# Optimization experiments

Measured on AMD Instinct MI355X. Metric: run time of the kernel, lower is better.

Reference implementation:

```python
import jax, jax.numpy as jnp
import numpy as np

NEG = -1e30


def setup_inputs() -> dict:
    key = jax.random.key(0)
    ks = jax.random.split(key, 8)
    B, d, Lc, Lq = 32, 128, 2048, 512
    C = jax.random.normal(ks[0], (B, d, Lc), dtype=jnp.float32)
    Q = jax.random.normal(ks[1], (B, d, Lq), dtype=jnp.float32)
    Cmask = jax.random.randint(ks[2], (B, Lc), 0, 2, dtype=jnp.int32)
    Qmask = jax.random.randint(ks[3], (B, Lq), 0, 2, dtype=jnp.int32)
    # xavier_uniform over (d, 1): bound = sqrt(6 / (d + 1))
    bnd = float(np.sqrt(6.0 / (d + 1)))
    w_c = jax.random.uniform(ks[4], (d, 1), minval=-bnd, maxval=bnd, dtype=jnp.float32)
    w_q = jax.random.uniform(ks[5], (d, 1), minval=-bnd, maxval=bnd, dtype=jnp.float32)
    bnd_m = float(np.sqrt(6.0 / (1 + d)))
    w_mul = jax.random.uniform(ks[6], (1, 1, d), minval=-bnd_m, maxval=bnd_m, dtype=jnp.float32)
    bias = jnp.zeros((1,), dtype=jnp.float32)
    return {"C": C, "Q": Q, "Cmask": Cmask, "Qmask": Qmask,
            "w_c": w_c, "w_q": w_q, "w_mul": w_mul, "bias": bias}


def reference(C, Q, Cmask, Qmask, w_c, w_q, w_mul, bias):
    # C: [B, d, Lc], Q: [B, d, Lq] -> transpose to token-major
    Ct = jnp.swapaxes(C, 1, 2)  # [B, Lc, d]
    Qt = jnp.swapaxes(Q, 1, 2)  # [B, Lq, d]
    cm = Cmask.astype(jnp.float32)[:, :, None]   # [B, Lc, 1]
    qm = Qmask.astype(jnp.float32)[:, None, :]   # [B, 1, Lq]
    # optimized trilinear similarity S: [B, Lc, Lq] (dropout p=0 / eval mode)
    s0 = Ct @ w_c                                  # [B, Lc, 1]
    s1 = jnp.swapaxes(Qt @ w_q, 1, 2)              # [B, 1, Lq]
    s2 = jnp.einsum('bcd,bqd->bcq', Ct * w_mul, Qt)  # [B, Lc, Lq]
    S = s0 + s1 + s2 + bias
    S1 = jax.nn.softmax(S + NEG * (1.0 - qm), axis=2)  # mask over query axis
    S2 = jax.nn.softmax(S + NEG * (1.0 - cm), axis=1)  # mask over context axis
    A = jnp.einsum('bcq,bqd->bcd', S1, Qt)             # [B, Lc, d]
    Bm = jnp.einsum('bck,bkd->bcd', jnp.einsum('bcq,bkq->bck', S1, S2), Ct)
    out = jnp.concatenate([Ct, A, Ct * A, Ct * Bm], axis=2)  # [B, Lc, 4d]
    return jnp.swapaxes(out, 1, 2)  # [B, 4d, Lc]
```

## Files before the change

### kernel.cpp

```cpp
#include <hip/hip_runtime.h>

#define B_ 32
#define D_ 128
#define LC 2048
#define LQ 512
#define CCH 16

#define NEGINF (-3.0e38f)

typedef __attribute__((ext_vector_type(8))) short bf16x8;
typedef __attribute__((ext_vector_type(4))) float f32x4;
typedef __attribute__((ext_vector_type(8))) unsigned short us8;
typedef __attribute__((ext_vector_type(8))) _Float16 f16x8;

__device__ __forceinline__ unsigned short bf16rne(float x) {
    unsigned int u = __float_as_uint(x);
    u = (u + 0x7FFFu + ((u >> 16) & 1u)) >> 16;
    return (unsigned short)u;
}

__device__ __forceinline__ void gll16(const void* g, void* l) {
    __builtin_amdgcn_global_load_lds((const __attribute__((address_space(1))) void*)g,
                                     (__attribute__((address_space(3))) void*)l, 16, 0, 0);
}

__global__ void k_dotw(const float* __restrict__ X, const float* __restrict__ w,
                       float* __restrict__ outv, int L) {
    int idx = blockIdx.x * 256 + threadIdx.x;
    int b = idx / L, x = idx - b * L;
    const float* Xp = X + (size_t)b * D_ * L + x;
    float acc = 0.f;
#pragma unroll 8
    for (int dd = 0; dd < D_; ++dd) acc += Xp[(size_t)dd * L] * w[dd];
    outv[idx] = acc;
}

__global__ void k_prep_C(const float* __restrict__ C, const float* __restrict__ wmul,
                         short* __restrict__ Ctw, short* __restrict__ Cb16) {
    int b = blockIdx.y, c0 = blockIdx.x * 64;
    __shared__ float Tf[128][65];
    __shared__ float wm[128];
    int t = threadIdx.x;
    if (t < 128) wm[t] = wmul[t];
    const float* Cb = C + (size_t)b * D_ * LC;
#pragma unroll
    for (int i = 0; i < 8; ++i) {
        int idx = t + i * 256;
        int d = idx >> 4, c4 = idx & 15;
        float4 v = *(const float4*)(Cb + (size_t)d * LC + c0 + c4 * 4);
        Tf[d][c4 * 4 + 0] = v.x; Tf[d][c4 * 4 + 1] = v.y;
        Tf[d][c4 * 4 + 2] = v.z; Tf[d][c4 * 4 + 3] = v.w;
        ushort4 cv;
        cv.x = bf16rne(v.x); cv.y = bf16rne(v.y); cv.z = bf16rne(v.z); cv.w = bf16rne(v.w);
        *(ushort4*)(Cb16 + ((size_t)b * D_ + d) * LC + c0 + c4 * 4) = cv;
    }
    __syncthreads();
    int c_l = t & 63, g = t >> 6;
    unsigned short u[32];
#pragma unroll
    for (int j = 0; j < 32; ++j) {
        int d = g * 32 + j;
        u[j] = bf16rne(Tf[d][c_l] * wm[d]);
    }
    short* dst = Ctw + ((size_t)b * LC + c0 + c_l) * D_ + g * 32;
#pragma unroll
    for (int k = 0; k < 4; ++k) *(us8*)(dst + k * 8) = *(const us8*)&u[k * 8];
}

__global__ void k_prep_Q(const float* __restrict__ Q, short* __restrict__ Qt16,
                         short* __restrict__ Wf) {
    int b = blockIdx.y, q0 = blockIdx.x * 64;
    __shared__ float Tf[128][65];
    int t = threadIdx.x;
    const float* Qb = Q + (size_t)b * D_ * LQ;
#pragma unroll
    for (int i = 0; i < 8; ++i) {
        int idx = t + i * 256;
        int d = idx >> 4, q4 = idx & 15;
        float4 v = *(const float4*)(Qb + (size_t)d * LQ + q0 + q4 * 4);
        Tf[d][q4 * 4 + 0] = v.x; Tf[d][q4 * 4 + 1] = v.y;
        Tf[d][q4 * 4 + 2] = v.z; Tf[d][q4 * 4 + 3] = v.w;
        ushort4 cv;
        cv.x = bf16rne(v.x); cv.y = bf16rne(v.y); cv.z = bf16rne(v.z); cv.w = bf16rne(v.w);
        *(ushort4*)(Wf + ((size_t)b * 256 + d) * LQ + q0 + q4 * 4) = cv;
    }
    __syncthreads();
    int q_l = t & 63, g = t >> 6;
    unsigned short u[32];
#pragma unroll
    for (int j = 0; j < 32; ++j) u[j] = bf16rne(Tf[g * 32 + j][q_l]);
    short* dst = Qt16 + ((size_t)b * LQ + q0 + q_l) * D_ + g * 32;
#pragma unroll
    for (int k = 0; k < 4; ++k) *(us8*)(dst + k * 8) = *(const us8*)&u[k * 8];
}

__global__ __launch_bounds__(256) void k_S_mfma(const short* __restrict__ Ctw,
                                                const short* __restrict__ Qt16,
                                                const float* __restrict__ s0,
                                                const float* __restrict__ s1,
                                                const float* __restrict__ bias,
                                                const int* __restrict__ Cmask,
                                                _Float16* __restrict__ S16,
                                                float* __restrict__ pm,
                                                float* __restrict__ pl) {
    int b = blockIdx.y;
    int cT = blockIdx.x >> 2, qT = blockIdx.x & 3;
    int c0 = cT * 128, q0 = qT * 128;
    int t = threadIdx.x, w = t >> 6, l = t & 63;
    int wm_ = w >> 1, wn = w & 1;
    __shared__ short As[128 * 64];
    __shared__ short Bs[128 * 64];
    f32x4 acc[4][4] = {};
    const short* Arow = Ctw + ((size_t)b * LC + c0) * D_;
    const short* Brow = Qt16 + ((size_t)b * LQ + q0) * D_;
    int lr = l >> 3, sl = l & 7;
    for (int kt = 0; kt < 2; ++kt) {
        __syncthreads();
#pragma unroll
        for (int i = 0; i < 4; ++i) {
            int r = w * 32 + i * 8 + lr;
            int g = sl ^ (r & 7);
            gll16(Arow + (size_t)r * D_ + kt * 64 + g * 8, &As[(w * 32 + i * 8) * 64]);
            gll16(Brow + (size_t)r * D_ + kt * 64 + g * 8, &Bs[(w * 32 + i * 8) * 64]);
        }
        __syncthreads();
#pragma unroll
        for (int ks = 0; ks < 2; ++ks) {
            int kg = ks * 4 + (l >> 4);
            bf16x8 af[4], bfr[4];
#pragma unroll
            for (int ms = 0; ms < 4; ++ms) {
                int m = wm_ * 64 + ms * 16 + (l & 15);
                af[ms] = *(const bf16x8*)&As[m * 64 + (kg ^ (m & 7)) * 8];
            }
#pragma unroll
            for (int ns = 0; ns < 4; ++ns) {
                int n = wn * 64 + ns * 16 + (l & 15);
                bfr[ns] = *(const bf16x8*)&Bs[n * 64 + (kg ^ (n & 7)) * 8];
            }
#pragma unroll
            for (int ms = 0; ms < 4; ++ms)
#pragma unroll
                for (int ns = 0; ns < 4; ++ns)
                    acc[ms][ns] = __builtin_amdgcn_mfma_f32_16x16x32_bf16(af[ms], bfr[ns], acc[ms][ns], 0, 0, 0);
        }
    }
    float bv = bias[0];
    float s0v[16];
    int cmv[16];
#pragma unroll
    for (int ms = 0; ms < 4; ++ms) {
        int cb = c0 + wm_ * 64 + ms * 16 + (l >> 4) * 4;
        float4 sv = *(const float4*)(s0 + b * LC + cb);
        s0v[ms * 4 + 0] = sv.x; s0v[ms * 4 + 1] = sv.y;
        s0v[ms * 4 + 2] = sv.z; s0v[ms * 4 + 3] = sv.w;
        int4 cv = *(const int4*)(Cmask + b * LC + cb);
        cmv[ms * 4 + 0] = cv.x; cmv[ms * 4 + 1] = cv.y;
        cmv[ms * 4 + 2] = cv.z; cmv[ms * 4 + 3] = cv.w;
    }
    __syncthreads();
    float* Mp = (float*)As;
    float* Lp = (float*)Bs;
    int prow = wm_ * 4 + (l >> 4);
#pragma unroll
    for (int ns = 0; ns < 4; ++ns) {
        int qi = wn * 64 + ns * 16 + (l & 15);
        int q = q0 + qi;
        float s1v = s1[b * LQ + q] + bv;
        float vq16[16];
#pragma unroll
        for (int ms = 0; ms < 4; ++ms) {
            int cb = c0 + wm_ * 64 + ms * 16 + (l >> 4) * 4;
#pragma unroll
            for (int r = 0; r < 4; ++r) {
                float vf = acc[ms][ns][r] + s0v[ms * 4 + r] + s1v;
                _Float16 h = (_Float16)vf;
                S16[((size_t)b * LC + cb + r) * LQ + q] = h;
                vq16[ms * 4 + r] = (float)h;
            }
        }
        float mt = NEGINF;
#pragma unroll
        for (int k = 0; k < 16; ++k) mt = fmaxf(mt, cmv[k] ? vq16[k] : NEGINF);
        float st = 0.f;
#pragma unroll
        for (int k = 0; k < 16; ++k) st += cmv[k] ? __expf(vq16[k] - mt) : 0.f;
        Mp[prow * 132 + qi] = mt;
        Lp[prow * 132 + qi] = st;
    }
    __syncthreads();
    if (t < 128) {
        float mm = Mp[t], ll = Lp[t];
#pragma unroll
        for (int g = 1; g < 8; ++g) {
            float m2 = Mp[g * 132 + t], l2 = Lp[g * 132 + t];
            float mn = fmaxf(mm, m2);
            ll = ll * __expf(mm - mn) + l2 * __expf(m2 - mn);
            mm = mn;
        }
        size_t o = ((size_t)cT * B_ + b) * LQ + q0 + t;
        pm[o] = mm; pl[o] = ll;
    }
}

__global__ void k_rowsoftmax(_Float16* __restrict__ S16, const int* __restrict__ Qmask) {
    int row = blockIdx.x * 4 + (threadIdx.x >> 6);
    int lane = threadIdx.x & 63;
    int b = row / LC;
    _Float16* Sp = S16 + (size_t)row * LQ + lane * 8;
    f16x8 v = *(const f16x8*)Sp;
    const int* qm = Qmask + b * LQ + lane * 8;
    int4 m0 = *(const int4*)qm;
    int4 m1 = *(const int4*)(qm + 4);
    int mk[8] = {m0.x, m0.y, m0.z, m0.w, m1.x, m1.y, m1.z, m1.w};
    float vf[8];
#pragma unroll
    for (int k = 0; k < 8; ++k) vf[k] = (float)v[k];
    float mx = NEGINF;
#pragma unroll
    for (int k = 0; k < 8; ++k) if (mk[k]) mx = fmaxf(mx, vf[k]);
#pragma unroll
    for (int off = 32; off > 0; off >>= 1) mx = fmaxf(mx, __shfl_xor(mx, off, 64));
    float e[8];
    float s = 0.f;
#pragma unroll
    for (int k = 0; k < 8; ++k) { e[k] = __expf(vf[k] - mx); if (mk[k]) s += e[k]; }
#pragma unroll
    for (int off = 32; off > 0; off >>= 1) s += __shfl_xor(s, off, 64);
    float ri = 1.0f / s;
    unsigned short u[8];
#pragma unroll
    for (int k = 0; k < 8; ++k) u[k] = mk[k] ? bf16rne(e[k] * ri) : (unsigned short)0;
    *(us8*)Sp = *(const us8*)&u[0];
}

__global__ void k_colstats_comb(const float* __restrict__ pm, const float* __restrict__ pl,
                                float* __restrict__ colmax, float* __restrict__ colsum) {
    int idx = blockIdx.x * 256 + threadIdx.x;
    float m = NEGINF, l = 0.f;
#pragma unroll
    for (int ch = 0; ch < CCH; ++ch) {
        float m2 = pm[(size_t)ch * B_ * LQ + idx];
        float l2 = pl[(size_t)ch * B_ * LQ + idx];
        float mn = fmaxf(m, m2);
        l = l * __expf(m - mn) + l2 * __expf(m2 - mn);
        m = mn;
    }
    colmax[idx] = m; colsum[idx] = l;
}

__global__ __launch_bounds__(256) void k_V2_mfma(const short* __restrict__ Cb16,
                                                 const _Float16* __restrict__ S16,
                                                 const int* __restrict__ Cmask,
                                                 const float* __restrict__ colmax,
                                                 const float* __restrict__ colsum,
                                                 short* __restrict__ Wf) {
    int b = blockIdx.y;
    int q0 = blockIdx.x * 64;
    int t = threadIdx.x, w = t >> 6, l = t & 63;
    __shared__ short As[128 * 64];
    __shared__ short Bs[64 * 72];
    f32x4 acc[2][4] = {};
    const short* Arow = Cb16 + (size_t)b * D_ * LC;
    int lr = l >> 3, sl = l & 7;
    float cmx[16];
#pragma unroll
    for (int j2 = 0; j2 < 4; ++j2)
        *(float4*)&cmx[j2 * 4] = *(const float4*)(colmax + b * LQ + q0 + w * 16 + j2 * 4);
    const _Float16* Sq = S16 + (size_t)b * LC * LQ + q0 + w * 16;
    const int* cmb = Cmask + b * LC;

    for (int kt = 0; kt < 32; ++kt) {
        int ck = kt * 64;
        __syncthreads();
#pragma unroll
        for (int i = 0; i < 4; ++i) {
            int r = w * 32 + i * 8 + lr;
            int g = sl ^ (r & 7);
            gll16(Arow + (size_t)r * LC + ck + g * 8, &As[(w * 32 + i * 8) * 64]);
        }
        {
            float cmf = (float)cmb[ck + l];
            const _Float16* sp = Sq + (size_t)(ck + l) * LQ;
            f16x8 v0 = *(const f16x8*)sp;
            f16x8 v1 = *(const f16x8*)(sp + 8);
#pragma unroll
            for (int j = 0; j < 8; ++j)
                Bs[(w * 16 + j) * 72 + l] = (short)bf16rne(cmf * __expf((float)v0[j] - cmx[j]));
#pragma unroll
            for (int j = 0; j < 8; ++j)
                Bs[(w * 16 + 8 + j) * 72 + l] = (short)bf16rne(cmf * __expf((float)v1[j] - cmx[8 + j]));
        }
        __syncthreads();
#pragma unroll
        for (int ks = 0; ks < 2; ++ks) {
            int kg = ks * 4 + (l >> 4);
            bf16x8 af[2], bfr[4];
#pragma unroll
            for (int ms = 0; ms < 2; ++ms) {
                int m = w * 32 + ms * 16 + (l & 15);
                af[ms] = *(const bf16x8*)&As[m * 64 + (kg ^ (m & 7)) * 8];
            }
#pragma unroll
            for (int ns = 0; ns < 4; ++ns) {
                int n = ns * 16 + (l & 15);
                bfr[ns] = *(const bf16x8*)&Bs[n * 72 + kg * 8];
            }
#pragma unroll
            for (int ms = 0; ms < 2; ++ms)
#pragma unroll
                for (int ns = 0; ns < 4; ++ns)
                    acc[ms][ns] = __builtin_amdgcn_mfma_f32_16x16x32_bf16(af[ms], bfr[ns], acc[ms][ns], 0, 0, 0);
        }
    }
#pragma unroll
    for (int ms = 0; ms < 2; ++ms)
#pragma unroll
        for (int ns = 0; ns < 4; ++ns) {
            int q = q0 + ns * 16 + (l & 15);
            float csi = 1.0f / colsum[b * LQ + q];
#pragma unroll
            for (int r = 0; r < 4; ++r) {
                int dd = w * 32 + ms * 16 + (l >> 4) * 4 + r;
                Wf[((size_t)b * 256 + 128 + dd) * LQ + q] = (short)bf16rne(acc[ms][ns][r] * csi);
            }
        }
}

__global__ __launch_bounds__(512) void k_out_mfma(const short* __restrict__ P1,
                                                  const short* __restrict__ Wf,
                                                  const float* __restrict__ C,
                                                  float* __restrict__ out) {
    int b = blockIdx.y;
    int c0 = blockIdx.x * 128;
    int t = threadIdx.x, w = t >> 6, l = t & 63;
    int wn = w & 3, wc = w >> 2;
    __shared__ short As[2 * 256 * 64];
    __shared__ short Bs[2 * 128 * 64];
    f32x4 acc[4][4] = {};
    const short* Arow = Wf + (size_t)b * 256 * LQ;
    const short* Brow = P1 + ((size_t)b * LC + c0) * LQ;
    int lr = l >> 3, sl = l & 7;
    int g = sl ^ lr;

#define STAGE(p, kt)                                                              \
    {                                                                             \
        short* Ad = As + (p) * (256 * 64);                                        \
        short* Bd = Bs + (p) * (128 * 64);                                        \
        _Pragma("unroll")                                                         \
        for (int i = 0; i < 4; ++i) {                                             \
            int r = w * 32 + i * 8 + lr;                                          \
            gll16(Arow + (size_t)r * LQ + (kt) * 64 + g * 8,                      \
                  &Ad[(w * 32 + i * 8) * 64]);                                    \
        }                                                                         \
        _Pragma("unroll")                                                         \
        for (int i = 0; i < 2; ++i) {                                             \
            int r = w * 16 + i * 8 + lr;                                          \
            gll16(Brow + (size_t)r * LQ + (kt) * 64 + g * 8,                      \
                  &Bd[(w * 16 + i * 8) * 64]);                                    \
        }                                                                         \
    }

    STAGE(0, 0);
    int cur = 0;
    for (int kt = 0; kt < 8; ++kt) {
        if (kt < 7) {
            STAGE(cur ^ 1, kt + 1);
            asm volatile("s_waitcnt vmcnt(6)" ::: "memory");
        } else {
            asm volatile("s_waitcnt vmcnt(0)" ::: "memory");
        }
        __builtin_amdgcn_s_barrier();
        __builtin_amdgcn_sched_barrier(0);
        const short* Ac = As + cur * (256 * 64);
        const short* Bc = Bs + cur * (128 * 64);
#pragma unroll
        for (int ks = 0; ks < 2; ++ks) {
            int kg = ks * 4 + (l >> 4);
            bf16x8 af[4], bfr[4];
#pragma unroll
            for (int ms = 0; ms < 4; ++ms) {
                int m = wn * 64 + ms * 16 + (l & 15);
                af[ms] = *(const bf16x8*)&Ac[m * 64 + (kg ^ (m & 7)) * 8];
            }
#pragma unroll
            for (int ns = 0; ns < 4; ++ns) {
                int cc = wc * 64 + ns * 16 + (l & 15);
                bfr[ns] = *(const bf16x8*)&Bc[cc * 64 + (kg ^ (cc & 7)) * 8];
            }
#pragma unroll
            for (int ms = 0; ms < 4; ++ms)
#pragma unroll
                for (int ns = 0; ns < 4; ++ns)
                    acc[ms][ns] = __builtin_amdgcn_mfma_f32_16x16x32_bf16(af[ms], bfr[ns], acc[ms][ns], 0, 0, 0);
        }
        __builtin_amdgcn_s_barrier();
        cur ^= 1;
    }
#undef STAGE
#pragma unroll
    for (int ms = 0; ms < 4; ++ms) {
        int nb = wn * 64 + ms * 16 + (l >> 4) * 4;
#pragma unroll
        for (int ns = 0; ns < 4; ++ns) {
            int c = c0 + wc * 64 + ns * 16 + (l & 15);
#pragma unroll
            for (int r = 0; r < 4; ++r) {
                int n = nb + r;
                float a = acc[ms][ns][r];
                if (n < 128) {
                    float cv = C[((size_t)b * D_ + n) * LC + c];
                    out[((size_t)b * 512 + n) * LC + c] = cv;
                    out[((size_t)b * 512 + 128 + n) * LC + c] = a;
                    out[((size_t)b * 512 + 256 + n) * LC + c] = cv * a;
                } else {
                    int dd = n - 128;
                    float cv = C[((size_t)b * D_ + dd) * LC + c];
                    out[((size_t)b * 512 + 384 + dd) * LC + c] = cv * a;
                }
            }
        }
    }
}

extern "C" void kernel_launch(void* const* d_in, const int* in_sizes, int n_in,
                              void* d_out, int out_size, void* d_ws, size_t ws_size,
                              hipStream_t stream) {
    const float* C     = (const float*)d_in[0];
    const float* Q     = (const float*)d_in[1];
    const int*   Cmask = (const int*)d_in[2];
    const int*   Qmask = (const int*)d_in[3];
    const float* w_c   = (const float*)d_in[4];
    const float* w_q   = (const float*)d_in[5];
    const float* w_mul = (const float*)d_in[6];
    const float* bias  = (const float*)d_in[7];
    float* out = (float*)d_out;

    _Float16* S16 = (_Float16*)d_ws;
    short* Cb16 = (short*)(S16 + (size_t)B_ * LC * LQ);
    short* Ctw  = Cb16 + (size_t)B_ * D_ * LC;
    short* Qt16 = Ctw + (size_t)B_ * LC * D_;
    short* Wf   = Qt16 + (size_t)B_ * LQ * D_;
    float* s0     = (float*)(Wf + (size_t)B_ * 256 * LQ);
    float* s1     = s0 + B_ * LC;
    float* colmax = s1 + B_ * LQ;
    float* colsum = colmax + B_ * LQ;
    float* pm     = colsum + B_ * LQ;
    float* pl     = pm + (size_t)CCH * B_ * LQ;

    hipLaunchKernelGGL(k_dotw, dim3(B_ * LC / 256), dim3(256), 0, stream, C, w_c, s0, LC);
    hipLaunchKernelGGL(k_dotw, dim3(B_ * LQ / 256), dim3(256), 0, stream, Q, w_q, s1, LQ);
    hipLaunchKernelGGL(k_prep_C, dim3(LC / 64, B_), dim3(256), 0, stream, C, w_mul, Ctw, Cb16);
    hipLaunchKernelGGL(k_prep_Q, dim3(LQ / 64, B_), dim3(256), 0, stream, Q, Qt16, Wf);
    hipLaunchKernelGGL(k_S_mfma, dim3((LC / 128) * (LQ / 128), B_), dim3(256), 0, stream,
                       Ctw, Qt16, s0, s1, bias, Cmask, S16, pm, pl);
    hipLaunchKernelGGL(k_colstats_comb, dim3(B_ * LQ / 256), dim3(256), 0, stream,
                       pm, pl, colmax, colsum);
    hipLaunchKernelGGL(k_V2_mfma, dim3(LQ / 64, B_), dim3(256), 0, stream,
                       Cb16, S16, Cmask, colmax, colsum, Wf);
    hipLaunchKernelGGL(k_rowsoftmax, dim3(B_ * LC / 4), dim3(256), 0, stream, S16, Qmask);
    hipLaunchKernelGGL(k_out_mfma, dim3(LC / 128, B_), dim3(512), 0, stream,
                       (const short*)S16, Wf, C, out);
}
```

Baseline: 389.9 us.

## Fuse row-softmax normalization into V2 kernel and restage out GEMM buffers

Measured after the change: 397.3 us. About the same (+1.9%).

```diff
diff --git a/kernel.cpp b/kernel.cpp
--- a/kernel.cpp
+++ b/kernel.cpp
@@ -203,12 +203,12 @@
     }
 }
 
-__global__ void k_rowsoftmax(_Float16* __restrict__ S16, const int* __restrict__ Qmask) {
+__global__ void k_rowstats(const _Float16* __restrict__ S16, const int* __restrict__ Qmask,
+                           float* __restrict__ rowmax, float* __restrict__ rowsum) {
     int row = blockIdx.x * 4 + (threadIdx.x >> 6);
     int lane = threadIdx.x & 63;
     int b = row / LC;
-    _Float16* Sp = S16 + (size_t)row * LQ + lane * 8;
-    f16x8 v = *(const f16x8*)Sp;
+    f16x8 v = *(const f16x8*)(S16 + (size_t)row * LQ + lane * 8);
     const int* qm = Qmask + b * LQ + lane * 8;
     int4 m0 = *(const int4*)qm;
     int4 m1 = *(const int4*)(qm + 4);
@@ -221,17 +221,12 @@
     for (int k = 0; k < 8; ++k) if (mk[k]) mx = fmaxf(mx, vf[k]);
 #pragma unroll
     for (int off = 32; off > 0; off >>= 1) mx = fmaxf(mx, __shfl_xor(mx, off, 64));
-    float e[8];
     float s = 0.f;
 #pragma unroll
-    for (int k = 0; k < 8; ++k) { e[k] = __expf(vf[k] - mx); if (mk[k]) s += e[k]; }
+    for (int k = 0; k < 8; ++k) if (mk[k]) s += __expf(vf[k] - mx);
 #pragma unroll
     for (int off = 32; off > 0; off >>= 1) s += __shfl_xor(s, off, 64);
-    float ri = 1.0f / s;
-    unsigned short u[8];
-#pragma unroll
-    for (int k = 0; k < 8; ++k) u[k] = mk[k] ? bf16rne(e[k] * ri) : (unsigned short)0;
-    *(us8*)Sp = *(const us8*)&u[0];
+    if (lane == 0) { rowmax[row] = mx; rowsum[row] = s; }
 }
 
 __global__ void k_colstats_comb(const float* __restrict__ pm, const float* __restrict__ pl,
@@ -250,10 +245,13 @@
 }
 
 __global__ __launch_bounds__(256) void k_V2_mfma(const short* __restrict__ Cb16,
-                                                 const _Float16* __restrict__ S16,
+                                                 _Float16* __restrict__ S16,
                                                  const int* __restrict__ Cmask,
+                                                 const int* __restrict__ Qmask,
                                                  const float* __restrict__ colmax,
                                                  const float* __restrict__ colsum,
+                                                 const float* __restrict__ rowmax,
+                                                 const float* __restrict__ rowsum,
                                                  short* __restrict__ Wf) {
     int b = blockIdx.y;
     int q0 = blockIdx.x * 64;
@@ -267,8 +265,14 @@
 #pragma unroll
     for (int j2 = 0; j2 < 4; ++j2)
         *(float4*)&cmx[j2 * 4] = *(const float4*)(colmax + b * LQ + q0 + w * 16 + j2 * 4);
-    const _Float16* Sq = S16 + (size_t)b * LC * LQ + q0 + w * 16;
+    int qmv[16];
+#pragma unroll
+    for (int j2 = 0; j2 < 4; ++j2)
+        *(int4*)&qmv[j2 * 4] = *(const int4*)(Qmask + b * LQ + q0 + w * 16 + j2 * 4);
+    _Float16* Sq = S16 + (size_t)b * LC * LQ + q0 + w * 16;
     const int* cmb = Cmask + b * LC;
+    const float* rmb = rowmax + b * LC;
+    const float* rsb = rowsum + b * LC;
 
     for (int kt = 0; kt < 32; ++kt) {
         int ck = kt * 64;
@@ -280,8 +284,11 @@
             gll16(Arow + (size_t)r * LC + ck + g * 8, &As[(w * 32 + i * 8) * 64]);
         }
         {
-            float cmf = (float)cmb[ck + l];
-            const _Float16* sp = Sq + (size_t)(ck + l) * LQ;
+            int c = ck + l;
+            float cmf = (float)cmb[c];
+            float rm = rmb[c];
+            float ri = 1.0f / rsb[c];
+            _Float16* sp = Sq + (size_t)c * LQ;
             f16x8 v0 = *(const f16x8*)sp;
             f16x8 v1 = *(const f16x8*)(sp + 8);
 #pragma unroll
@@ -290,6 +297,15 @@
 #pragma unroll
             for (int j = 0; j < 8; ++j)
                 Bs[(w * 16 + 8 + j) * 72 + l] = (short)bf16rne(cmf * __expf((float)v1[j] - cmx[8 + j]));
+            unsigned short p0[8], p1r[8];
+#pragma unroll
+            for (int j = 0; j < 8; ++j)
+                p0[j] = qmv[j] ? bf16rne(__expf((float)v0[j] - rm) * ri) : (unsigned short)0;
+#pragma unroll
+            for (int j = 0; j < 8; ++j)
+                p1r[j] = qmv[8 + j] ? bf16rne(__expf((float)v1[j] - rm) * ri) : (unsigned short)0;
+            *(us8*)sp = *(const us8*)&p0[0];
+            *(us8*)(sp + 8) = *(const us8*)&p1r[0];
         }
         __syncthreads();
 #pragma unroll
@@ -336,44 +352,43 @@
     int t = threadIdx.x, w = t >> 6, l = t & 63;
     int wn = w & 3, wc = w >> 2;
     __shared__ short As[2 * 256 * 64];
-    __shared__ short Bs[2 * 128 * 64];
+    __shared__ short Bs[128 * 64];
     f32x4 acc[4][4] = {};
     const short* Arow = Wf + (size_t)b * 256 * LQ;
     const short* Brow = P1 + ((size_t)b * LC + c0) * LQ;
     int lr = l >> 3, sl = l & 7;
     int g = sl ^ lr;
 
-#define STAGE(p, kt)                                                              \
+#define STAGE_A(p, kt)                                                            \
     {                                                                             \
         short* Ad = As + (p) * (256 * 64);                                        \
-        short* Bd = Bs + (p) * (128 * 64);                                        \
         _Pragma("unroll")                                                         \
         for (int i = 0; i < 4; ++i) {                                             \
             int r = w * 32 + i * 8 + lr;                                          \
             gll16(Arow + (size_t)r * LQ + (kt) * 64 + g * 8,                      \
                   &Ad[(w * 32 + i * 8) * 64]);                                    \
         }                                                                         \
+    }
+#define STAGE_B(kt)                                                               \
+    {                                                                             \
         _Pragma("unroll")                                                         \
         for (int i = 0; i < 2; ++i) {                                             \
             int r = w * 16 + i * 8 + lr;                                          \
             gll16(Brow + (size_t)r * LQ + (kt) * 64 + g * 8,                      \
-                  &Bd[(w * 16 + i * 8) * 64]);                                    \
+                  &Bs[(w * 16 + i * 8) * 64]);                                    \
         }                                                                         \
     }
 
-    STAGE(0, 0);
+    STAGE_B(0);
+    STAGE_A(0, 0);
+    STAGE_A(1, 1);
     int cur = 0;
     for (int kt = 0; kt < 8; ++kt) {
-        if (kt < 7) {
-            STAGE(cur ^ 1, kt + 1);
-            asm volatile("s_waitcnt vmcnt(6)" ::: "memory");
-        } else {
-            asm volatile("s_waitcnt vmcnt(0)" ::: "memory");
-        }
+        if (kt < 7) asm volatile("s_waitcnt vmcnt(4)" ::: "memory");
+        else        asm volatile("s_waitcnt vmcnt(0)" ::: "memory");
         __builtin_amdgcn_s_barrier();
         __builtin_amdgcn_sched_barrier(0);
         const short* Ac = As + cur * (256 * 64);
-        const short* Bc = Bs + cur * (128 * 64);
 #pragma unroll
         for (int ks = 0; ks < 2; ++ks) {
             int kg = ks * 4 + (l >> 4);
@@ -386,7 +401,7 @@
 #pragma unroll
             for (int ns = 0; ns < 4; ++ns) {
                 int cc = wc * 64 + ns * 16 + (l & 15);
-                bfr[ns] = *(const bf16x8*)&Bc[cc * 64 + (kg ^ (cc & 7)) * 8];
+                bfr[ns] = *(const bf16x8*)&Bs[cc * 64 + (kg ^ (cc & 7)) * 8];
             }
 #pragma unroll
             for (int ms = 0; ms < 4; ++ms)
@@ -395,9 +410,15 @@
                     acc[ms][ns] = __builtin_amdgcn_mfma_f32_16x16x32_bf16(af[ms], bfr[ns], acc[ms][ns], 0, 0, 0);
         }
         __builtin_amdgcn_s_barrier();
+        __builtin_amdgcn_sched_barrier(0);
+        if (kt < 7) {
+            STAGE_B(kt + 1);
+            if (kt < 6) STAGE_A(cur, kt + 2);
+        }
         cur ^= 1;
     }
-#undef STAGE
+#undef STAGE_A
+#undef STAGE_B
 #pragma unroll
     for (int ms = 0; ms < 4; ++ms) {
         int nb = wn * 64 + ms * 16 + (l >> 4) * 4;
@@ -445,7 +466,9 @@
     float* s1     = s0 + B_ * LC;
     float* colmax = s1 + B_ * LQ;
     float* colsum = colmax + B_ * LQ;
-    float* pm     = colsum + B_ * LQ;
+    float* rowmax = colsum + B_ * LQ;
+    float* rowsum = rowmax + B_ * LC;
+    float* pm     = rowsum + B_ * LC;
     float* pl     = pm + (size_t)CCH * B_ * LQ;
 
     hipLaunchKernelGGL(k_dotw, dim3(B_ * LC / 256), dim3(256), 0, stream, C, w_c, s0, LC);
@@ -456,9 +479,9 @@
                        Ctw, Qt16, s0, s1, bias, Cmask, S16, pm, pl);
     hipLaunchKernelGGL(k_colstats_comb, dim3(B_ * LQ / 256), dim3(256), 0, stream,
                        pm, pl, colmax, colsum);
+    hipLaunchKernelGGL(k_rowstats, dim3(B_ * LC / 4), dim3(256), 0, stream, S16, Qmask, rowmax, rowsum);
     hipLaunchKernelGGL(k_V2_mfma, dim3(LQ / 64, B_), dim3(256), 0, stream,
-                       Cb16, S16, Cmask, colmax, colsum, Wf);
-    hipLaunchKernelGGL(k_rowsoftmax, dim3(B_ * LC / 4), dim3(256), 0, stream, S16, Qmask);
+                       Cb16, S16, Cmask, Qmask, colmax, colsum, rowmax, rowsum, Wf);
     hipLaunchKernelGGL(k_out_mfma, dim3(LC / 128, B_), dim3(512), 0, stream,
                        (const short*)S16, Wf, C, out);
 }
```
